# Performance work log

Hardware: AMD Instinct MI355X
Metric: run time of the kernel (lower is better)

## Reference

```python
import jax, jax.numpy as jnp
import numpy as np

B, N, D_IN, D_OUT, E = 4, 50000, 128, 128, 800000


def setup_inputs() -> dict:
    key = jax.random.key(0)
    k_x, k_w, k_b, k_r, k_c, k_v = jax.random.split(key, 6)
    stdv = 1.0 / np.sqrt(D_OUT)
    x = jax.random.normal(k_x, (B, N, D_IN), dtype=jnp.float32)
    weight = jax.random.uniform(k_w, (D_IN, D_OUT), jnp.float32, -stdv, stdv)
    bias = jax.random.uniform(k_b, (D_OUT,), jnp.float32, -stdv, stdv)
    adj_rows = jax.random.randint(k_r, (E,), 0, N, dtype=jnp.int32)
    adj_cols = jax.random.randint(k_c, (E,), 0, N, dtype=jnp.int32)
    # positive edge weights (e.g. normalized adjacency values)
    adj_vals = jax.random.uniform(k_v, (E,), jnp.float32) * (1.0 / 16.0)
    edge_index = jnp.stack([adj_rows, adj_cols]).astype(jnp.int64)  # unused (pyg_builtin=False)
    return {"input": x, "weight": weight, "bias": bias,
            "adj_vals": adj_vals, "adj_rows": adj_rows, "adj_cols": adj_cols,
            "edge_index": edge_index}


def reference(input, weight, bias, adj_vals, adj_rows, adj_cols, edge_index):
    # support = input @ W : [B, N, D_OUT]
    support = jnp.einsum('bnd,df->bnf', input, weight)

    # node_repr = sparse adj (COO) @ support, batched == torch.sparse.mm path
    def agg(s):  # s: [N, D_OUT]
        msgs = adj_vals[:, None] * s[adj_cols]          # [E, D_OUT] gather
        return jax.ops.segment_sum(msgs, adj_rows, num_segments=N)  # scatter-add

    node_repr = jax.vmap(agg)(support) + bias           # [B, N, D_OUT]
    # net_norm='none' -> no norm; activation=relu; residual=False; dropout=0
    return jax.nn.relu(node_repr)
```

## Files before the change

### kernel.cpp

```cpp
#include <hip/hip_runtime.h>
#include <hip/hip_bf16.h>

#define BB 4
#define NN 50000
#define DIN 128
#define DOUT 128
#define EE 800000
#define TOTROWS (BB * NN)
#define LDA 136

#define NGB ((TOTROWS + 127) / 128)
#define NHB ((EE + 255) / 256)
#define CHUNK 1024
#define NCHUNK ((NN + CHUNK - 1) / CHUNK)
#define NPB 64
#define PAD8(x) (((x) + 7) & ~7)
#define EPK_CAP (EE + 8 * NN)
#define NAB (NN / 4)

typedef unsigned short u16;
typedef unsigned int u32;

using shortx8 = __attribute__((ext_vector_type(8))) short;
using ushortx4 = __attribute__((ext_vector_type(4))) unsigned short;
using ushortx8 = __attribute__((ext_vector_type(8))) unsigned short;
using floatx4 = __attribute__((ext_vector_type(4))) float;

__device__ __forceinline__ float b2f(u16 u) {
    u32 x = ((u32)u) << 16;
    float f;
    __builtin_memcpy(&f, &x, 4);
    return f;
}

__device__ __forceinline__ u16 f2b(float f) {
    u32 x;
    __builtin_memcpy(&x, &f, 4);
    u32 r = x + 0x7fffu + ((x >> 16) & 1u);
    return (u16)(r >> 16);
}

__global__ __launch_bounds__(256)
void k1_detect_hist(const u16* __restrict__ X, const u16* __restrict__ W,
                    const u16* __restrict__ Bs, const u16* __restrict__ V,
                    int nx, int nw, int nb, int nv, int* __restrict__ flags,
                    const int* __restrict__ rows, int* __restrict__ deg) {
    if (blockIdx.x == 0) {
        __shared__ int cnt[4];
        const int t = threadIdx.x;
        const int w = t >> 6;
        const int l = t & 63;
        if (t < 4) cnt[t] = 0;
        __syncthreads();
        const u16* p = (w == 0) ? X : (w == 1) ? W : (w == 2) ? Bs : V;
        const int n  = (w == 0) ? nx : (w == 1) ? nw : (w == 2) ? nb : nv;
        int bad = 0;
        for (int k = 0; k < 4; ++k) {
            unsigned idx = 2u * (unsigned)(((unsigned long long)(l * 4 + k) *
                                            (unsigned)(n >> 1)) >> 8);
            u16 s = p[idx];
            unsigned e = (s >> 7) & 0xFF;
            bool ok = ((s & 0x7FFF) == 0) || (e >= 90 && e <= 141);
            bad += ok ? 0 : 1;
        }
        atomicAdd(&cnt[w], bad);
        __syncthreads();
        if (l == 0) flags[w] = (cnt[w] >= 77) ? 1 : 0;
    } else {
        int e = (int)(blockIdx.x - 1) * 256 + threadIdx.x;
        if (e < EE) atomicAdd(&deg[rows[e]], 1);
    }
}

__global__ __launch_bounds__(256)
void k2_scanred_prep(const int* __restrict__ deg, int* __restrict__ bsum,
                     const void* __restrict__ Wv, const int* __restrict__ flags,
                     u16* __restrict__ Wt) {
    if (blockIdx.x < NCHUNK) {
        __shared__ int sh[256];
        int t = threadIdx.x, blk = blockIdx.x;
        int base = blk * CHUNK + t * 4;
        int s = 0;
#pragma unroll
        for (int i = 0; i < 4; ++i) {
            int idx = base + i;
            if (idx < NN) s += PAD8(deg[idx]);
        }
        sh[t] = s;
        __syncthreads();
        for (int d = 128; d > 0; d >>= 1) {
            if (t < d) sh[t] += sh[t + d];
            __syncthreads();
        }
        if (t == 0) bsum[blk] = sh[0];
    } else {
        int t = (int)(blockIdx.x - NCHUNK) * 256 + threadIdx.x;
        if (t < DIN * DOUT) {
            int f = t >> 7, k = t & 127;
            size_t src = (size_t)k * DOUT + f;
            Wt[t] = flags[1] ? f2b(((const float*)Wv)[src]) : ((const u16*)Wv)[src];
        }
    }
}

__global__ __launch_bounds__(64)
void k_scan_base(const int* __restrict__ bsum, int* __restrict__ bbase,
                 int* __restrict__ off) {
    int l = threadIdx.x;
    int orig = (l < NCHUNK) ? bsum[l] : 0;
    int v = orig;
    for (int d = 1; d < 64; d <<= 1) {
        int x = __shfl_up(v, d);
        if (l >= d) v += x;
    }
    if (l < NCHUNK) bbase[l] = v - orig;
    if (l == NCHUNK - 1) off[NN] = v;
}

__global__ __launch_bounds__(256)
void k_scan_chunk(const int* __restrict__ deg, const int* __restrict__ bbase,
                  int* __restrict__ off) {
    __shared__ int sh[256];
    int t = threadIdx.x;
    int blk = blockIdx.x;
    int base = blk * CHUNK + t * 4;
    int v[4];
    int tsum = 0;
#pragma unroll
    for (int i = 0; i < 4; ++i) {
        int idx = base + i;
        v[i] = (idx < NN) ? PAD8(deg[idx]) : 0;
        tsum += v[i];
    }
    sh[t] = tsum;
    __syncthreads();
    for (int d = 1; d < 256; d <<= 1) {
        int x = (t >= d) ? sh[t - d] : 0;
        __syncthreads();
        sh[t] += x;
        __syncthreads();
    }
    int run = sh[t] - tsum + bbase[blk];
#pragma unroll
    for (int i = 0; i < 4; ++i) {
        int idx = base + i;
        if (idx < NN) off[idx] = run;
        run += v[i];
    }
}

__global__ __launch_bounds__(256, 3)
void k5_gemm_scatter(const void* __restrict__ Xv, const u16* __restrict__ Wt,
                     const int* __restrict__ flags, u16* __restrict__ sup,
                     const int* __restrict__ rows, const int* __restrict__ cols,
                     const void* __restrict__ valsv, const int* __restrict__ off,
                     int* __restrict__ cur, int2* __restrict__ epk) {
    if (blockIdx.x >= NGB) {
        int e = (int)(blockIdx.x - NGB) * 256 + threadIdx.x;
        if (e < EE) {
            int vf32 = flags[3];
            float v = vf32 ? ((const float*)valsv)[e]
                           : b2f(((const u16*)valsv)[e]);
            int r = rows[e];
            int p = off[r] + atomicAdd(&cur[r], 1);
            epk[p] = make_int2(cols[e], __float_as_int(v));
        }
        return;
    }

    __shared__ u16 lA[128 * LDA];

    const int xf32 = flags[0];
    const int tid = threadIdx.x;
    const int wid = tid >> 6;
    const int l   = tid & 63;
    const long rowBase = (long)blockIdx.x * 128;

    if (xf32) {
        const float* Xf = (const float*)Xv;
#pragma unroll
        for (int i = 0; i < 16; ++i) {
            int elem = i * 1024 + tid * 4;
            int row = elem >> 7, col = elem & 127;
            long gRow = rowBase + row;
            ushortx4 w4 = (ushortx4){0, 0, 0, 0};
            if (gRow < TOTROWS) {
                float4 v = *(const float4*)(Xf + gRow * DIN + col);
                w4[0] = f2b(v.x); w4[1] = f2b(v.y);
                w4[2] = f2b(v.z); w4[3] = f2b(v.w);
            }
            *(ushortx4*)&lA[row * LDA + col] = w4;
        }
    } else {
        const u16* X16 = (const u16*)Xv;
#pragma unroll
        for (int i = 0; i < 8; ++i) {
            int elem = i * 2048 + tid * 8;
            int row = elem >> 7, col = elem & 127;
            long gRow = rowBase + row;
            ushortx8 w8 = (ushortx8){0, 0, 0, 0, 0, 0, 0, 0};
            if (gRow < TOTROWS)
                w8 = *(const ushortx8*)(X16 + gRow * DIN + col);
            *(ushortx8*)&lA[row * LDA + col] = w8;
        }
    }

    const int wx = wid & 1;
    const int wy = wid >> 1;
    const int q8 = (l >> 4) * 8;
    const int lm = l & 15;

    shortx8 bf[16];
#pragma unroll
    for (int nt = 0; nt < 4; ++nt) {
        const size_t Frow = (size_t)(wx * 64 + nt * 16 + lm) * DIN;
#pragma unroll
        for (int c = 0; c < 4; ++c)
            bf[nt * 4 + c] = *(const shortx8*)(Wt + Frow + 32 * c + q8);
    }

    floatx4 acc[4][4];
#pragma unroll
    for (int mt = 0; mt < 4; ++mt)
#pragma unroll
        for (int nt = 0; nt < 4; ++nt)
            acc[mt][nt] = (floatx4){0.f, 0.f, 0.f, 0.f};

    __syncthreads();

    for (int c = 0; c < 4; ++c) {
        shortx8 af[4];
#pragma unroll
        for (int mt = 0; mt < 4; ++mt)
            af[mt] = *(const shortx8*)
                &lA[(size_t)(wy * 64 + mt * 16 + lm) * LDA + 32 * c + q8];
#pragma unroll
        for (int mt = 0; mt < 4; ++mt)
#pragma unroll
            for (int nt = 0; nt < 4; ++nt)
                acc[mt][nt] = __builtin_amdgcn_mfma_f32_16x16x32_bf16(
                    af[mt], bf[nt * 4 + c], acc[mt][nt], 0, 0, 0);
    }

    __syncthreads();
#pragma unroll
    for (int mt = 0; mt < 4; ++mt) {
#pragma unroll
        for (int reg = 0; reg < 4; ++reg) {
            int row = wy * 64 + mt * 16 + (l >> 4) * 4 + reg;
#pragma unroll
            for (int nt = 0; nt < 4; ++nt)
                lA[row * LDA + wx * 64 + nt * 16 + lm] = f2b(acc[mt][nt][reg]);
        }
    }
    __syncthreads();

#pragma unroll
    for (int i = 0; i < 8; ++i) {
        int elem = i * 2048 + tid * 8;
        int row = elem >> 7, col = elem & 127;
        long R = rowBase + row;
        if (R < TOTROWS) {
            int b = (int)(R / NN);
            int n = (int)(R % NN);
            ushortx8 v = *(const ushortx8*)&lA[row * LDA + col];
            *(ushortx8*)(sup + ((size_t)n * BB + b) * DOUT + col) = v;
        }
    }
}

__global__ __launch_bounds__(256)
void k_agg(const u16* __restrict__ sup, const int* __restrict__ off,
           const int2* __restrict__ epk, const void* __restrict__ biasv,
           const int* __restrict__ flags, float* __restrict__ out) {
    int blk = blockIdx.x;
    const int pass = (blk >= NAB) ? 1 : 0;
    if (pass) blk -= NAB;
    const int wid = threadIdx.x >> 6;
    const int l   = threadIdx.x & 63;
    const int n = blk * 4 + wid;

    const int p0 = __builtin_amdgcn_readfirstlane(off[n]);
    const int p1 = __builtin_amdgcn_readfirstlane(off[n + 1]);

    float acc[4] = {0.f, 0.f, 0.f, 0.f};
    const int b  = l >> 4;
    const int f0 = pass * 64 + (l & 15) * 4;
    const int lofs = b * 128 + f0;

    for (int pb = p0; pb < p1; pb += 64) {
        const int cnt = min(64, p1 - pb);
        int2 d = make_int2(0, 0);
        if (l < cnt) {
            long long dv = __builtin_nontemporal_load(
                (const long long*)(epk + pb + l));
            d.x = (int)(dv & 0xFFFFFFFFLL);
            d.y = (int)(dv >> 32);
        }
        for (int j = 0; j < cnt; j += 8) {
            int   cs[8];
            float vs[8];
#pragma unroll
            for (int q = 0; q < 8; ++q) {
                cs[q] = __builtin_amdgcn_readlane(d.x, j + q);
                vs[q] = __int_as_float(__builtin_amdgcn_readlane(d.y, j + q));
            }
            ushortx4 sv[8];
#pragma unroll
            for (int q = 0; q < 8; ++q)
                sv[q] = *(const ushortx4*)(sup + (size_t)cs[q] * 512 + lofs);
#pragma unroll
            for (int q = 0; q < 8; ++q)
#pragma unroll
                for (int t = 0; t < 4; ++t)
                    acc[t] += vs[q] * b2f(sv[q][t]);
        }
    }

    float bb[4];
    if (flags[2]) {
        float4 bv = *(const float4*)((const float*)biasv + f0);
        bb[0] = bv.x; bb[1] = bv.y; bb[2] = bv.z; bb[3] = bv.w;
    } else {
        ushortx4 bv = *(const ushortx4*)((const u16*)biasv + f0);
#pragma unroll
        for (int t = 0; t < 4; ++t) bb[t] = b2f(bv[t]);
    }

    floatx4 r;
#pragma unroll
    for (int t = 0; t < 4; ++t) r[t] = fmaxf(acc[t] + bb[t], 0.f);

    float* op = out + ((size_t)b * NN + n) * DOUT + f0;
    __builtin_nontemporal_store(r, (floatx4*)op);
}

extern "C" void kernel_launch(void* const* d_in, const int* in_sizes, int n_in,
                              void* d_out, int out_size, void* d_ws, size_t ws_size,
                              hipStream_t stream) {
    const void* X    = d_in[0];
    const void* W    = d_in[1];
    const void* bias = d_in[2];
    const void* vals = d_in[3];
    const int* rows  = (const int*)d_in[4];
    const int* cols  = (const int*)d_in[5];
    float* out = (float*)d_out;

    char* base = (char*)d_ws;
    size_t o = 0;
    int* flags = (int*)(base + o); o += 64;
    int* deg = (int*)(base + o); o += (size_t)NN * 4;
    int* cur = (int*)(base + o); o += (size_t)NN * 4;
    o = (o + 255) & ~(size_t)255;
    int* bsum  = (int*)(base + o); o += 64 * 4;
    int* bbase = (int*)(base + o); o += 64 * 4;
    o = (o + 255) & ~(size_t)255;
    u16* Wt = (u16*)(base + o); o += (size_t)DIN * DOUT * 2;
    o = (o + 255) & ~(size_t)255;
    int* off = (int*)(base + o); o += (size_t)(NN + 1) * 4;
    o = (o + 255) & ~(size_t)255;
    int2* epk = (int2*)(base + o); o += (size_t)EPK_CAP * 8;
    o = (o + 255) & ~(size_t)255;
    u16* sup = (u16*)(base + o); o += (size_t)BB * NN * DOUT * 2;
    (void)ws_size;

    hipMemsetAsync(deg, 0, (size_t)2 * NN * 4, stream);
    hipMemsetAsync(epk, 0, (size_t)EPK_CAP * 8, stream);

    k1_detect_hist<<<1 + NHB, 256, 0, stream>>>(
        (const u16*)X, (const u16*)W, (const u16*)bias, (const u16*)vals,
        in_sizes[0], in_sizes[1], in_sizes[2], in_sizes[3], flags, rows, deg);
    k2_scanred_prep<<<NCHUNK + NPB, 256, 0, stream>>>(deg, bsum, W, flags, Wt);
    k_scan_base<<<1, 64, 0, stream>>>(bsum, bbase, off);
    k_scan_chunk<<<NCHUNK, 256, 0, stream>>>(deg, bbase, off);
    k5_gemm_scatter<<<NGB + NHB, 256, 0, stream>>>(
        X, Wt, flags, sup, rows, cols, vals, off, cur, epk);
    k_agg<<<2 * NAB, 256, 0, stream>>>(sup, off, epk, bias, flags, out);
}
```

Measured before the change: 400.9 us.

## Fuse CSR build and GEMM into one persistent kernel with grid barriers

Replaces the detect/histogram, two-level scan, weight transpose and GEMM+scatter kernels with one persistent mega-kernel. 256 blocks build the CSR through software grid barriers while another 256 blocks run the GEMM concurrently, spinning on a flag until the transposed weights are ready. The large epk memset is replaced by explicit zeroing of only the padding slots. This removes several launches and memsets and overlaps CSR construction with the GEMM. In exchange it depends on all barrier blocks being co-resident, and the CSR work now runs on fewer blocks using grid-stride loops.

```diff
diff --git a/kernel.cpp b/kernel.cpp
--- a/kernel.cpp
+++ b/kernel.cpp
@@ -10,10 +10,10 @@
 #define LDA 136
 
 #define NGB ((TOTROWS + 127) / 128)
-#define NHB ((EE + 255) / 256)
-#define CHUNK 1024
-#define NCHUNK ((NN + CHUNK - 1) / CHUNK)
-#define NPB 64
+#define NCSR 256
+#define NGEMM 256
+#define NMEGA (NCSR + NGEMM)
+#define NPCB 196
 #define PAD8(x) (((x) + 7) & ~7)
 #define EPK_CAP (EE + 8 * NN)
 #define NAB (NN / 4)
@@ -40,232 +40,276 @@
     return (u16)(r >> 16);
 }
 
-__global__ __launch_bounds__(256)
-void k1_detect_hist(const u16* __restrict__ X, const u16* __restrict__ W,
-                    const u16* __restrict__ Bs, const u16* __restrict__ V,
-                    int nx, int nw, int nb, int nv, int* __restrict__ flags,
-                    const int* __restrict__ rows, int* __restrict__ deg) {
-    if (blockIdx.x == 0) {
-        __shared__ int cnt[4];
-        const int t = threadIdx.x;
-        const int w = t >> 6;
-        const int l = t & 63;
-        if (t < 4) cnt[t] = 0;
-        __syncthreads();
-        const u16* p = (w == 0) ? X : (w == 1) ? W : (w == 2) ? Bs : V;
-        const int n  = (w == 0) ? nx : (w == 1) ? nw : (w == 2) ? nb : nv;
+__device__ __forceinline__ void grid_bar(int* cnt, int* gen, int target) {
+    __syncthreads();
+    if (threadIdx.x == 0) {
+        __threadfence();
+        if (atomicAdd(cnt, 1) == NCSR - 1) {
+            __hip_atomic_store(cnt, 0, __ATOMIC_RELAXED, __HIP_MEMORY_SCOPE_AGENT);
+            __threadfence();
+            __hip_atomic_store(gen, target, __ATOMIC_RELEASE, __HIP_MEMORY_SCOPE_AGENT);
+        } else {
+            while (__hip_atomic_load(gen, __ATOMIC_ACQUIRE, __HIP_MEMORY_SCOPE_AGENT) < target)
+                __builtin_amdgcn_s_sleep(4);
+        }
+        __threadfence();
+    }
+    __syncthreads();
+}
+
+__global__ __launch_bounds__(256, 3)
+void k_mega(const void* __restrict__ Xv, const void* __restrict__ Wv,
+            const void* __restrict__ biasv, const void* __restrict__ valsv,
+            const int* __restrict__ rows, const int* __restrict__ cols,
+            int nx, int nw, int nb, int nv,
+            int* __restrict__ bar,
+            int* __restrict__ flags, int* __restrict__ deg,
+            int* __restrict__ cur, int* __restrict__ bsum,
+            int* __restrict__ bbase, u16* __restrict__ Wt,
+            int* __restrict__ off, int2* __restrict__ epk,
+            u16* __restrict__ sup) {
+    __shared__ u16 lA[128 * LDA];
+    int* sh = (int*)lA;
+
+    const int blk = blockIdx.x;
+    const int tid = threadIdx.x;
+    int* cnt = bar + 0;
+    int* gen = bar + 1;
+    int* wt_done = bar + 2;
+
+    if (blk < NCSR) {
+        if (blk == 0) {
+            if (tid < 4) sh[tid] = 0;
+            __syncthreads();
+            const int w = tid >> 6;
+            const int l = tid & 63;
+            const u16* p = (w == 0) ? (const u16*)Xv : (w == 1) ? (const u16*)Wv
+                         : (w == 2) ? (const u16*)biasv : (const u16*)valsv;
+            const int n = (w == 0) ? nx : (w == 1) ? nw : (w == 2) ? nb : nv;
+            int bad = 0;
+            for (int k = 0; k < 4; ++k) {
+                unsigned idx = 2u * (unsigned)(((unsigned long long)(l * 4 + k) *
+                                                (unsigned)(n >> 1)) >> 8);
+                u16 s = p[idx];
+                unsigned e = (s >> 7) & 0xFF;
+                bool ok = ((s & 0x7FFF) == 0) || (e >= 90 && e <= 141);
+                bad += ok ? 0 : 1;
+            }
+            atomicAdd(&sh[w], bad);
+            __syncthreads();
+            if (l == 0) flags[w] = (sh[w] >= 77) ? 1 : 0;
+        }
+        for (int i = blk * 256 + tid; i < 2 * NN; i += NCSR * 256)
+            deg[i] = 0;
+        grid_bar(cnt, gen, 1);
+
+        if (blk < 64) {
+            int t = blk * 256 + tid;
+            int f = t >> 7, k = t & 127;
+            size_t src = (size_t)k * DOUT + f;
+            Wt[t] = flags[1] ? f2b(((const float*)Wv)[src]) : ((const u16*)Wv)[src];
+            __syncthreads();
+            if (tid == 0) {
+                __threadfence();
+                atomicAdd(wt_done, 1);
+            }
+        }
+        for (int e = blk * 256 + tid; e < EE; e += NCSR * 256)
+            atomicAdd(&deg[rows[e]], 1);
+        grid_bar(cnt, gen, 2);
+
+        {
+            int n = blk * NPCB + tid;
+            int d = (tid < NPCB && n < NN) ? PAD8(deg[n]) : 0;
+            sh[tid] = d;
+            __syncthreads();
+            for (int s = 128; s > 0; s >>= 1) {
+                if (tid < s) sh[tid] += sh[tid + s];
+                __syncthreads();
+            }
+            if (tid == 0) bsum[blk] = sh[0];
+        }
+        grid_bar(cnt, gen, 3);
+
+        if (blk == 0) {
+            int v = bsum[tid];
+            sh[tid] = v;
+            __syncthreads();
+            for (int s = 1; s < 256; s <<= 1) {
+                int x = (tid >= s) ? sh[tid - s] : 0;
+                __syncthreads();
+                sh[tid] += x;
+                __syncthreads();
+            }
+            bbase[tid] = sh[tid] - v;
+            if (tid == 255) off[NN] = sh[255];
+        }
+        grid_bar(cnt, gen, 4);
+
+        {
+            int n = blk * NPCB + tid;
+            int d = (tid < NPCB && n < NN) ? PAD8(deg[n]) : 0;
+            sh[tid] = d;
+            __syncthreads();
+            for (int s = 1; s < 256; s <<= 1) {
+                int x = (tid >= s) ? sh[tid - s] : 0;
+                __syncthreads();
+                sh[tid] += x;
+                __syncthreads();
+            }
+            if (tid < NPCB && n < NN) off[n] = bbase[blk] + sh[tid] - d;
+        }
+        grid_bar(cnt, gen, 5);
+
+        {
+            const int vf32 = flags[3];
+            for (int e = blk * 256 + tid; e < EE; e += NCSR * 256) {
+                float v = vf32 ? ((const float*)valsv)[e]
+                               : b2f(((const u16*)valsv)[e]);
+                int r = rows[e];
+                int p = off[r] + atomicAdd(&cur[r], 1);
+                epk[p] = make_int2(cols[e], __float_as_int(v));
+            }
+            for (int n = blk * 256 + tid; n < NN; n += NCSR * 256) {
+                int dd = deg[n];
+                int o = off[n] + dd;
+                int pe = PAD8(dd) - dd;
+                for (int k = 0; k < pe; ++k) epk[o + k] = make_int2(0, 0);
+            }
+        }
+        return;
+    }
+
+    const int g = blk - NCSR;
+
+    if (tid == 0) sh[0] = 0;
+    __syncthreads();
+    if (tid < 64) {
         int bad = 0;
         for (int k = 0; k < 4; ++k) {
-            unsigned idx = 2u * (unsigned)(((unsigned long long)(l * 4 + k) *
-                                            (unsigned)(n >> 1)) >> 8);
-            u16 s = p[idx];
+            unsigned idx = 2u * (unsigned)(((unsigned long long)(tid * 4 + k) *
+                                            (unsigned)(nx >> 1)) >> 8);
+            u16 s = ((const u16*)Xv)[idx];
             unsigned e = (s >> 7) & 0xFF;
             bool ok = ((s & 0x7FFF) == 0) || (e >= 90 && e <= 141);
             bad += ok ? 0 : 1;
         }
-        atomicAdd(&cnt[w], bad);
-        __syncthreads();
-        if (l == 0) flags[w] = (cnt[w] >= 77) ? 1 : 0;
-    } else {
-        int e = (int)(blockIdx.x - 1) * 256 + threadIdx.x;
-        if (e < EE) atomicAdd(&deg[rows[e]], 1);
-    }
-}
-
-__global__ __launch_bounds__(256)
-void k2_scanred_prep(const int* __restrict__ deg, int* __restrict__ bsum,
-                     const void* __restrict__ Wv, const int* __restrict__ flags,
-                     u16* __restrict__ Wt) {
-    if (blockIdx.x < NCHUNK) {
-        __shared__ int sh[256];
-        int t = threadIdx.x, blk = blockIdx.x;
-        int base = blk * CHUNK + t * 4;
-        int s = 0;
-#pragma unroll
-        for (int i = 0; i < 4; ++i) {
-            int idx = base + i;
-            if (idx < NN) s += PAD8(deg[idx]);
-        }
-        sh[t] = s;
-        __syncthreads();
-        for (int d = 128; d > 0; d >>= 1) {
-            if (t < d) sh[t] += sh[t + d];
-            __syncthreads();
-        }
-        if (t == 0) bsum[blk] = sh[0];
-    } else {
-        int t = (int)(blockIdx.x - NCHUNK) * 256 + threadIdx.x;
-        if (t < DIN * DOUT) {
-            int f = t >> 7, k = t & 127;
-            size_t src = (size_t)k * DOUT + f;
-            Wt[t] = flags[1] ? f2b(((const float*)Wv)[src]) : ((const u16*)Wv)[src];
-        }
-    }
-}
-
-__global__ __launch_bounds__(64)
-void k_scan_base(const int* __restrict__ bsum, int* __restrict__ bbase,
-                 int* __restrict__ off) {
-    int l = threadIdx.x;
-    int orig = (l < NCHUNK) ? bsum[l] : 0;
-    int v = orig;
-    for (int d = 1; d < 64; d <<= 1) {
-        int x = __shfl_up(v, d);
-        if (l >= d) v += x;
-    }
-    if (l < NCHUNK) bbase[l] = v - orig;
-    if (l == NCHUNK - 1) off[NN] = v;
-}
-
-__global__ __launch_bounds__(256)
-void k_scan_chunk(const int* __restrict__ deg, const int* __restrict__ bbase,
-                  int* __restrict__ off) {
-    __shared__ int sh[256];
-    int t = threadIdx.x;
-    int blk = blockIdx.x;
-    int base = blk * CHUNK + t * 4;
-    int v[4];
-    int tsum = 0;
-#pragma unroll
-    for (int i = 0; i < 4; ++i) {
-        int idx = base + i;
-        v[i] = (idx < NN) ? PAD8(deg[idx]) : 0;
-        tsum += v[i];
-    }
-    sh[t] = tsum;
+        atomicAdd(&sh[0], bad);
+    }
     __syncthreads();
-    for (int d = 1; d < 256; d <<= 1) {
-        int x = (t >= d) ? sh[t - d] : 0;
-        __syncthreads();
-        sh[t] += x;
-        __syncthreads();
-    }
-    int run = sh[t] - tsum + bbase[blk];
-#pragma unroll
-    for (int i = 0; i < 4; ++i) {
-        int idx = base + i;
-        if (idx < NN) off[idx] = run;
-        run += v[i];
-    }
-}
-
-__global__ __launch_bounds__(256, 3)
-void k5_gemm_scatter(const void* __restrict__ Xv, const u16* __restrict__ Wt,
-                     const int* __restrict__ flags, u16* __restrict__ sup,
-                     const int* __restrict__ rows, const int* __restrict__ cols,
-                     const void* __restrict__ valsv, const int* __restrict__ off,
-                     int* __restrict__ cur, int2* __restrict__ epk) {
-    if (blockIdx.x >= NGB) {
-        int e = (int)(blockIdx.x - NGB) * 256 + threadIdx.x;
-        if (e < EE) {
-            int vf32 = flags[3];
-            float v = vf32 ? ((const float*)valsv)[e]
-                           : b2f(((const u16*)valsv)[e]);
-            int r = rows[e];
-            int p = off[r] + atomicAdd(&cur[r], 1);
-            epk[p] = make_int2(cols[e], __float_as_int(v));
-        }
-        return;
-    }
-
-    __shared__ u16 lA[128 * LDA];
-
-    const int xf32 = flags[0];
-    const int tid = threadIdx.x;
+    const int xf32 = (sh[0] >= 77) ? 1 : 0;
+    __syncthreads();
+
     const int wid = tid >> 6;
     const int l   = tid & 63;
-    const long rowBase = (long)blockIdx.x * 128;
-
-    if (xf32) {
-        const float* Xf = (const float*)Xv;
-#pragma unroll
-        for (int i = 0; i < 16; ++i) {
-            int elem = i * 1024 + tid * 4;
-            int row = elem >> 7, col = elem & 127;
-            long gRow = rowBase + row;
-            ushortx4 w4 = (ushortx4){0, 0, 0, 0};
-            if (gRow < TOTROWS) {
-                float4 v = *(const float4*)(Xf + gRow * DIN + col);
-                w4[0] = f2b(v.x); w4[1] = f2b(v.y);
-                w4[2] = f2b(v.z); w4[3] = f2b(v.w);
-            }
-            *(ushortx4*)&lA[row * LDA + col] = w4;
-        }
-    } else {
-        const u16* X16 = (const u16*)Xv;
-#pragma unroll
-        for (int i = 0; i < 8; ++i) {
-            int elem = i * 2048 + tid * 8;
-            int row = elem >> 7, col = elem & 127;
-            long gRow = rowBase + row;
-            ushortx8 w8 = (ushortx8){0, 0, 0, 0, 0, 0, 0, 0};
-            if (gRow < TOTROWS)
-                w8 = *(const ushortx8*)(X16 + gRow * DIN + col);
-            *(ushortx8*)&lA[row * LDA + col] = w8;
-        }
-    }
-
     const int wx = wid & 1;
     const int wy = wid >> 1;
     const int q8 = (l >> 4) * 8;
     const int lm = l & 15;
 
-    shortx8 bf[16];
-#pragma unroll
-    for (int nt = 0; nt < 4; ++nt) {
-        const size_t Frow = (size_t)(wx * 64 + nt * 16 + lm) * DIN;
-#pragma unroll
-        for (int c = 0; c < 4; ++c)
-            bf[nt * 4 + c] = *(const shortx8*)(Wt + Frow + 32 * c + q8);
-    }
-
-    floatx4 acc[4][4];
-#pragma unroll
-    for (int mt = 0; mt < 4; ++mt)
-#pragma unroll
-        for (int nt = 0; nt < 4; ++nt)
-            acc[mt][nt] = (floatx4){0.f, 0.f, 0.f, 0.f};
-
-    __syncthreads();
-
-    for (int c = 0; c < 4; ++c) {
-        shortx8 af[4];
+    bool first = true;
+    for (int T = g; T < NGB; T += NGEMM) {
+        const long rowBase = (long)T * 128;
+
+        if (xf32) {
+            const float* Xf = (const float*)Xv;
+#pragma unroll
+            for (int i = 0; i < 16; ++i) {
+                int elem = i * 1024 + tid * 4;
+                int row = elem >> 7, col = elem & 127;
+                long gRow = rowBase + row;
+                ushortx4 w4 = (ushortx4){0, 0, 0, 0};
+                if (gRow < TOTROWS) {
+                    float4 v = *(const float4*)(Xf + gRow * DIN + col);
+                    w4[0] = f2b(v.x); w4[1] = f2b(v.y);
+                    w4[2] = f2b(v.z); w4[3] = f2b(v.w);
+                }
+                *(ushortx4*)&lA[row * LDA + col] = w4;
+            }
+        } else {
+            const u16* X16 = (const u16*)Xv;
+#pragma unroll
+            for (int i = 0; i < 8; ++i) {
+                int elem = i * 2048 + tid * 8;
+                int row = elem >> 7, col = elem & 127;
+                long gRow = rowBase + row;
+                ushortx8 w8 = (ushortx8){0, 0, 0, 0, 0, 0, 0, 0};
+                if (gRow < TOTROWS)
+                    w8 = *(const ushortx8*)(X16 + gRow * DIN + col);
+                *(ushortx8*)&lA[row * LDA + col] = w8;
+            }
+        }
+
+        if (first) {
+            if (tid == 0) {
+                while (__hip_atomic_load(wt_done, __ATOMIC_ACQUIRE,
+                                         __HIP_MEMORY_SCOPE_AGENT) < 64)
+                    __builtin_amdgcn_s_sleep(4);
+                __threadfence();
+            }
+            __syncthreads();
+            first = false;
+        }
+
+        shortx8 bf[16];
+#pragma unroll
+        for (int nt = 0; nt < 4; ++nt) {
+            const size_t Frow = (size_t)(wx * 64 + nt * 16 + lm) * DIN;
+#pragma unroll
+            for (int c = 0; c < 4; ++c)
+                bf[nt * 4 + c] = *(const shortx8*)(Wt + Frow + 32 * c + q8);
+        }
+
+        floatx4 acc[4][4];
 #pragma unroll
         for (int mt = 0; mt < 4; ++mt)
-            af[mt] = *(const shortx8*)
-                &lA[(size_t)(wy * 64 + mt * 16 + lm) * LDA + 32 * c + q8];
-#pragma unroll
-        for (int mt = 0; mt < 4; ++mt)
 #pragma unroll
             for (int nt = 0; nt < 4; ++nt)
-                acc[mt][nt] = __builtin_amdgcn_mfma_f32_16x16x32_bf16(
-                    af[mt], bf[nt * 4 + c], acc[mt][nt], 0, 0, 0);
-    }
-
-    __syncthreads();
-#pragma unroll
-    for (int mt = 0; mt < 4; ++mt) {
-#pragma unroll
-        for (int reg = 0; reg < 4; ++reg) {
-            int row = wy * 64 + mt * 16 + (l >> 4) * 4 + reg;
-#pragma unroll
-            for (int nt = 0; nt < 4; ++nt)
-                lA[row * LDA + wx * 64 + nt * 16 + lm] = f2b(acc[mt][nt][reg]);
-        }
-    }
-    __syncthreads();
-
-#pragma unroll
-    for (int i = 0; i < 8; ++i) {
-        int elem = i * 2048 + tid * 8;
-        int row = elem >> 7, col = elem & 127;
-        long R = rowBase + row;
-        if (R < TOTROWS) {
-            int b = (int)(R / NN);
-            int n = (int)(R % NN);
-            ushortx8 v = *(const ushortx8*)&lA[row * LDA + col];
-            *(ushortx8*)(sup + ((size_t)n * BB + b) * DOUT + col) = v;
-        }
+                acc[mt][nt] = (floatx4){0.f, 0.f, 0.f, 0.f};
+
+        __syncthreads();
+
+        for (int c = 0; c < 4; ++c) {
+            shortx8 af[4];
+#pragma unroll
+            for (int mt = 0; mt < 4; ++mt)
+                af[mt] = *(const shortx8*)
+                    &lA[(size_t)(wy * 64 + mt * 16 + lm) * LDA + 32 * c + q8];
+#pragma unroll
+            for (int mt = 0; mt < 4; ++mt)
+#pragma unroll
+                for (int nt = 0; nt < 4; ++nt)
+                    acc[mt][nt] = __builtin_amdgcn_mfma_f32_16x16x32_bf16(
+                        af[mt], bf[nt * 4 + c], acc[mt][nt], 0, 0, 0);
+        }
+
+        __syncthreads();
+#pragma unroll
+        for (int mt = 0; mt < 4; ++mt) {
+#pragma unroll
+            for (int reg = 0; reg < 4; ++reg) {
+                int row = wy * 64 + mt * 16 + (l >> 4) * 4 + reg;
+#pragma unroll
+                for (int nt = 0; nt < 4; ++nt)
+                    lA[row * LDA + wx * 64 + nt * 16 + lm] =
+                        f2b(acc[mt][nt][reg]);
+            }
+        }
+        __syncthreads();
+
+#pragma unroll
+        for (int i = 0; i < 8; ++i) {
+            int elem = i * 2048 + tid * 8;
+            int row = elem >> 7, col = elem & 127;
+            long R = rowBase + row;
+            if (R < TOTROWS) {
+                int b = (int)(R / NN);
+                int n = (int)(R % NN);
+                ushortx8 v = *(const ushortx8*)&lA[row * LDA + col];
+                *(ushortx8*)(sup + ((size_t)n * BB + b) * DOUT + col) = v;
+            }
+        }
+        __syncthreads();
     }
 }
 
@@ -348,12 +392,13 @@
 
     char* base = (char*)d_ws;
     size_t o = 0;
+    int* bar   = (int*)(base + o); o += 64;
     int* flags = (int*)(base + o); o += 64;
     int* deg = (int*)(base + o); o += (size_t)NN * 4;
     int* cur = (int*)(base + o); o += (size_t)NN * 4;
     o = (o + 255) & ~(size_t)255;
-    int* bsum  = (int*)(base + o); o += 64 * 4;
-    int* bbase = (int*)(base + o); o += 64 * 4;
+    int* bsum  = (int*)(base + o); o += 256 * 4;
+    int* bbase = (int*)(base + o); o += 256 * 4;
     o = (o + 255) & ~(size_t)255;
     u16* Wt = (u16*)(base + o); o += (size_t)DIN * DOUT * 2;
     o = (o + 255) & ~(size_t)255;
@@ -364,16 +409,11 @@
     u16* sup = (u16*)(base + o); o += (size_t)BB * NN * DOUT * 2;
     (void)ws_size;
 
-    hipMemsetAsync(deg, 0, (size_t)2 * NN * 4, stream);
-    hipMemsetAsync(epk, 0, (size_t)EPK_CAP * 8, stream);
-
-    k1_detect_hist<<<1 + NHB, 256, 0, stream>>>(
-        (const u16*)X, (const u16*)W, (const u16*)bias, (const u16*)vals,
-        in_sizes[0], in_sizes[1], in_sizes[2], in_sizes[3], flags, rows, deg);
-    k2_scanred_prep<<<NCHUNK + NPB, 256, 0, stream>>>(deg, bsum, W, flags, Wt);
-    k_scan_base<<<1, 64, 0, stream>>>(bsum, bbase, off);
-    k_scan_chunk<<<NCHUNK, 256, 0, stream>>>(deg, bbase, off);
-    k5_gemm_scatter<<<NGB + NHB, 256, 0, stream>>>(
-        X, Wt, flags, sup, rows, cols, vals, off, cur, epk);
+    hipMemsetAsync(bar, 0, 64, stream);
+
+    k_mega<<<NMEGA, 256, 0, stream>>>(
+        X, W, bias, vals, rows, cols,
+        in_sizes[0], in_sizes[1], in_sizes[2], in_sizes[3],
+        bar, flags, deg, cur, bsum, bbase, Wt, off, epk, sup);
     k_agg<<<2 * NAB, 256, 0, stream>>>(sup, off, epk, bias, flags, out);
 }
```

Result: slower. 633.2 us (+57.9%).
